# Kernel tuning notes

Hardware: AMD Instinct MI355X
Metric: run time of the kernel (lower is better)

Reference implementation:

```python
import jax, jax.numpy as jnp
import numpy as np

NUM_HEADS = 16
HEAD_DIM = 64
SCALE = 8.0 / HEAD_DIM  # use_mup=True
HGT, WID = 32, 32
EPS = 1e-5


def _layernorm(t, gamma, beta):
    # LayerNorm over last dim (head_dim)
    mu = jnp.mean(t, axis=-1, keepdims=True)
    var = jnp.var(t, axis=-1, keepdims=True)
    return (t - mu) * jax.lax.rsqrt(var + EPS) * gamma + beta


def _attention_1d(x, Wqkv, gamma, beta):
    # x: [B, N, C]; Wqkv: [3C, C] (torch Linear: y = x @ W.T)
    B, N, C = x.shape
    qkv = jnp.einsum('bnc,dc->bnd', x, Wqkv)                 # [B, N, 3C]
    qkv = qkv.reshape(B, N, 3, NUM_HEADS, HEAD_DIM)
    qkv = jnp.transpose(qkv, (2, 0, 3, 1, 4))                # [3, B, h, N, d]
    q, k, v = qkv[0], qkv[1], qkv[2]
    q = _layernorm(q, gamma, beta)
    k = _layernorm(k, gamma, beta)
    attn = jnp.einsum('bhnd,bhmd->bhnm', q * SCALE, k)       # [B, h, N, N]
    attn = jax.nn.softmax(attn, axis=-1)
    out = jnp.einsum('bhnm,bhmd->bhnd', attn, v)             # [B, h, N, d]
    return jnp.transpose(out, (0, 2, 1, 3)).reshape(B, N, C)


def setup_inputs() -> dict:
    key = jax.random.key(0)
    ks = jax.random.split(key, 3)
    B, N, C = 16, HGT * WID, 1024
    x = jax.random.normal(ks[0], (B, N, C), dtype=jnp.float32)
    Wqkv_row = jax.random.normal(ks[1], (3 * C, C), dtype=jnp.float32) * (1.0 / np.sqrt(C))
    Wqkv_col = jax.random.normal(ks[2], (3 * C, C), dtype=jnp.float32) * (1.0 / np.sqrt(C))
    return {
        'x': x,
        'Wqkv_row': Wqkv_row,
        'Wqkv_col': Wqkv_col,
        'gamma_row': jnp.ones((HEAD_DIM,), jnp.float32),
        'beta_row': jnp.zeros((HEAD_DIM,), jnp.float32),
        'gamma_col': jnp.ones((HEAD_DIM,), jnp.float32),
        'beta_col': jnp.zeros((HEAD_DIM,), jnp.float32),
    }


def reference(x, Wqkv_row, Wqkv_col, gamma_row, beta_row, gamma_col, beta_col):
    B, N, C = x.shape
    H, W = HGT, WID
    x2d = x.reshape(B, H, W, C)
    # Row attention: attend along W for every row; batch all rows together.
    rows = x2d.reshape(B * H, W, C)
    rows = _attention_1d(rows, Wqkv_row, gamma_row, beta_row)
    x2d = rows.reshape(B, H, W, C)
    # Column attention: attend along H for every column.
    cols = jnp.transpose(x2d, (0, 2, 1, 3)).reshape(B * W, H, C)
    cols = _attention_1d(cols, Wqkv_col, gamma_col, beta_col)
    x2d = jnp.transpose(cols.reshape(B, W, H, C), (0, 2, 1, 3))
    return x2d.reshape(B, N, C)
```

## Files before the change

kernel.cpp:

```cpp
#include <hip/hip_runtime.h>
#include <hip/hip_bf16.h>
#include <cstdint>

typedef _Float16 f16x8 __attribute__((ext_vector_type(8)));
typedef _Float16 f16x2 __attribute__((ext_vector_type(2)));
typedef float  f32x4  __attribute__((ext_vector_type(4)));
typedef unsigned short u16x8 __attribute__((ext_vector_type(8)));

#define GLDS(gp, lp) __builtin_amdgcn_global_load_lds( \
    (const __attribute__((address_space(1))) void*)(gp), \
    (__attribute__((address_space(3))) void*)(lp), 16, 0, 0)

static constexpr int   MROWS = 16384;
static constexpr int   N3    = 3072;
static constexpr int   NT    = 16;
static constexpr float SCALE = 0.125f;

#if __has_builtin(__builtin_amdgcn_fdot2)
#define FDOT2(a, b, c) __builtin_amdgcn_fdot2((a), (b), (c), false)
#else
__device__ __forceinline__ float FDOT2(f16x2 a, f16x2 b, float c) {
  return c + (float)a[0] * (float)b[0] + (float)a[1] * (float)b[1];
}
#endif

__device__ __forceinline__ unsigned short f2h_u(float f) {
  union { _Float16 h; unsigned short u; } c; c.h = (_Float16)f; return c.u;
}
__device__ __forceinline__ float h2f(unsigned short u) {
  union { unsigned short u; _Float16 h; } c; c.u = u; return (float)c.h;
}
__device__ __forceinline__ int permrow(int m) {
  return (m & ~1023) | ((m & 31) << 5) | ((m >> 5) & 31);
}

__global__ __launch_bounds__(256) void split_h(const float* __restrict__ src,
                                               unsigned short* __restrict__ dst) {
  int idx = blockIdx.x * 256 + threadIdx.x;
  int m = idx >> 7, k8 = (idx & 127) << 3;
  const float* s = src + (size_t)m * 1024 + k8;
  float4 v0 = *(const float4*)s;
  float4 v1 = *(const float4*)(s + 4);
  float vals[8] = {v0.x, v0.y, v0.z, v0.w, v1.x, v1.y, v1.z, v1.w};
  u16x8 hi;
#pragma unroll
  for (int i = 0; i < 8; ++i) hi[i] = f2h_u(vals[i]);
  *(u16x8*)(dst + (size_t)m * 1024 + k8) = hi;
}

__global__ __launch_bounds__(512, 2) void gemm256(const unsigned short* __restrict__ A,
                                                  const unsigned short* __restrict__ Bm,
                                                  unsigned short* __restrict__ Cq) {
  __shared__ unsigned char smem[131072];
  const int tid = threadIdx.x;
  const int w = tid >> 6, l = tid & 63;
  const int wr = w >> 2, wc = w & 3;

  const int bid = blockIdx.x;
  const int xcd = bid & 7, ic = bid >> 3;
  const int m0 = (xcd * 8 + ic / 12) << 8;
  const int n0 = (ic % 12) << 8;

  const int ske = ((l & 3) * 8) ^ ((l >= 32) ? 16 : 0);
  const unsigned short* gA0 = A  + (size_t)(m0 + w * 32 + (l >> 2)) * 1024 + ske;
  const unsigned short* gA1 = gA0 + 16 * 1024;
  const unsigned short* gB0 = Bm + (size_t)(n0 + w * 32 + (l >> 2)) * 1024 + ske;
  const unsigned short* gB1 = gB0 + 16 * 1024;
  int kT = 0;

  const int lr = l & 15;
  const int laneoff = ((lr * 64) + ((l >> 4) * 16)) ^ ((lr & 8) << 2);

#define STAGE_A(pb, kk) do { \
    GLDS(gA0 + kT + (kk) * 32, smem + (pb) * 65536 + (4 * w + (kk)) * 1024); \
    GLDS(gA1 + kT + (kk) * 32, smem + (pb) * 65536 + (4 * w + 2 + (kk)) * 1024); } while (0)
#define STAGE_B(pb, kk) do { \
    GLDS(gB0 + kT + (kk) * 32, smem + (pb) * 65536 + 32768 + (4 * w + (kk)) * 1024); \
    GLDS(gB1 + kT + (kk) * 32, smem + (pb) * 65536 + 32768 + (4 * w + 2 + (kk)) * 1024); } while (0)
#define MFMA(af, bf, c) __builtin_amdgcn_mfma_f32_16x16x32_f16(af, bf, c, 0, 0, 0)

  f32x4 acc[8][4] = {};

  STAGE_A(0, 0); STAGE_B(0, 0); STAGE_A(0, 1); STAGE_B(0, 1);
  kT = 64;
  asm volatile("s_waitcnt vmcnt(0)" ::: "memory");
  __builtin_amdgcn_s_barrier();

  for (int t = 0; t < NT; ++t) {
    const int p = t & 1, q = p ^ 1;
    const unsigned char* rb = smem + p * 65536;

    if (t < NT - 1) { STAGE_A(q, 0); STAGE_B(q, 0); STAGE_A(q, 1); STAGE_B(q, 1); }

#pragma unroll
    for (int kk = 0; kk < 2; ++kk) {
      const unsigned char* rk = rb + kk * 1024;
      f16x8 a[8], b[4];
#pragma unroll
      for (int mi = 0; mi < 8; ++mi)
        a[mi] = *(const f16x8*)(rk + (wr * 8 + mi) * 2048 + laneoff);
#pragma unroll
      for (int ni = 0; ni < 4; ++ni)
        b[ni] = *(const f16x8*)(rk + 32768 + (wc * 4 + ni) * 2048 + laneoff);
#pragma unroll
      for (int mi = 0; mi < 8; ++mi)
#pragma unroll
        for (int ni = 0; ni < 4; ++ni)
          acc[mi][ni] = MFMA(a[mi], b[ni], acc[mi][ni]);
    }

    if (t < NT - 1) {
      asm volatile("s_waitcnt vmcnt(0)" ::: "memory");
      __builtin_amdgcn_s_barrier();
    }
    kT += 64;
  }

  const int rq = (l >> 4) * 4;
#pragma unroll
  for (int mi = 0; mi < 8; ++mi)
#pragma unroll
    for (int ni = 0; ni < 4; ++ni) {
      int row = m0 + wr * 128 + mi * 16 + rq;
      int col = n0 + wc * 64 + ni * 16 + lr;
      unsigned short* cp = Cq + (size_t)row * N3 + col;
#pragma unroll
      for (int r = 0; r < 4; ++r)
        cp[(size_t)r * N3] = f2h_u(acc[mi][ni][r]);
    }
#undef STAGE_A
#undef STAGE_B
#undef MFMA
}

__global__ __launch_bounds__(256) void attn(const unsigned short* __restrict__ qkv,
                                            const float* __restrict__ gamma,
                                            const float* __restrict__ beta,
                                            float* __restrict__ out,
                                            unsigned short* __restrict__ a2,
                                            int mode) {
  __shared__ _Float16 qh[32][72];
  __shared__ _Float16 kh[32][72];
  __shared__ float v[32][68];
  __shared__ float pr[32][36];
  const int tid = threadIdx.x;
  const int s = blockIdx.x >> 4, hd = blockIdx.x & 15;
  const int p = tid >> 3, d0 = (tid & 7) * 8;
  const size_t base = (size_t)s * 32 * 3072 + hd * 64;

  {
    size_t r = base + (size_t)p * 3072 + d0;
    u16x8 qa = *(const u16x8*)(qkv + r);
    u16x8 ka = *(const u16x8*)(qkv + r + 1024);
    u16x8 va = *(const u16x8*)(qkv + r + 2048);
    float qf[8], kf[8];
    float q1 = 0.f, q2 = 0.f, k1 = 0.f, k2 = 0.f;
#pragma unroll
    for (int j = 0; j < 8; ++j) {
      qf[j] = h2f(qa[j]); kf[j] = h2f(ka[j]);
      q1 += qf[j]; q2 += qf[j] * qf[j];
      k1 += kf[j]; k2 += kf[j] * kf[j];
    }
#pragma unroll
    for (int m = 1; m <= 4; m <<= 1) {
      q1 += __shfl_xor(q1, m); q2 += __shfl_xor(q2, m);
      k1 += __shfl_xor(k1, m); k2 += __shfl_xor(k2, m);
    }
    float muq = q1 * 0.015625f, muk = k1 * 0.015625f;
    float rsq = rsqrtf(q2 * 0.015625f - muq * muq + 1e-5f);
    float rsk = rsqrtf(k2 * 0.015625f - muk * muk + 1e-5f);
    f32x4 g0 = *(const f32x4*)(gamma + d0);
    f32x4 g1 = *(const f32x4*)(gamma + d0 + 4);
    f32x4 b0 = *(const f32x4*)(beta + d0);
    f32x4 b1 = *(const f32x4*)(beta + d0 + 4);
    f16x8 qn16, kn16;
    f32x4 vv0, vv1;
#pragma unroll
    for (int j = 0; j < 8; ++j) {
      float gg = (j < 4) ? g0[j] : g1[j - 4];
      float bb = (j < 4) ? b0[j] : b1[j - 4];
      qn16[j] = (_Float16)(((qf[j] - muq) * rsq * gg + bb) * SCALE);
      kn16[j] = (_Float16)((kf[j] - muk) * rsk * gg + bb);
    }
#pragma unroll
    for (int j = 0; j < 4; ++j) { vv0[j] = h2f(va[j]); vv1[j] = h2f(va[4 + j]); }
    *(f16x8*)&qh[p][d0] = qn16;
    *(f16x8*)&kh[p][d0] = kn16;
    *(f32x4*)&v[p][d0]     = vv0;
    *(f32x4*)&v[p][d0 + 4] = vv1;
  }
  __syncthreads();

  {
    const int c0 = (tid & 7) * 4;
    float a0 = 0.f, a1 = 0.f, a2f = 0.f, a3 = 0.f;
#pragma unroll
    for (int dc = 0; dc < 8; ++dc) {
      union { f16x8 v8; f16x2 p2[4]; } qa, k0, k1, k2, k3;
      qa.v8 = *(const f16x8*)&qh[p][dc * 8];
      k0.v8 = *(const f16x8*)&kh[c0 + 0][dc * 8];
      k1.v8 = *(const f16x8*)&kh[c0 + 1][dc * 8];
      k2.v8 = *(const f16x8*)&kh[c0 + 2][dc * 8];
      k3.v8 = *(const f16x8*)&kh[c0 + 3][dc * 8];
#pragma unroll
      for (int j = 0; j < 4; ++j) {
        a0  = FDOT2(qa.p2[j], k0.p2[j], a0);
        a1  = FDOT2(qa.p2[j], k1.p2[j], a1);
        a2f = FDOT2(qa.p2[j], k2.p2[j], a2f);
        a3  = FDOT2(qa.p2[j], k3.p2[j], a3);
      }
    }
    f32x4 res; res[0] = a0; res[1] = a1; res[2] = a2f; res[3] = a3;
    *(f32x4*)&pr[p][c0] = res;
  }
  __syncthreads();

  {
    const int c0 = (tid & 7) * 4;
    f32x4 e = *(const f32x4*)&pr[p][c0];
    float mx = fmaxf(fmaxf(e[0], e[1]), fmaxf(e[2], e[3]));
#pragma unroll
    for (int m = 1; m <= 4; m <<= 1) mx = fmaxf(mx, __shfl_xor(mx, m));
    e[0] = __expf(e[0] - mx); e[1] = __expf(e[1] - mx);
    e[2] = __expf(e[2] - mx); e[3] = __expf(e[3] - mx);
    float sum = e[0] + e[1] + e[2] + e[3];
#pragma unroll
    for (int m = 1; m <= 4; m <<= 1) sum += __shfl_xor(sum, m);
    float inv = 1.f / sum;
    e[0] *= inv; e[1] *= inv; e[2] *= inv; e[3] *= inv;
    *(f32x4*)&pr[p][c0] = e;
  }
  __syncthreads();

  {
    f32x4 prr[8];
#pragma unroll
    for (int jq = 0; jq < 8; ++jq) prr[jq] = *(const f32x4*)&pr[p][jq * 4];
    f32x4 o0 = {0.f, 0.f, 0.f, 0.f}, o1 = {0.f, 0.f, 0.f, 0.f};
#pragma unroll
    for (int j = 0; j < 32; ++j) {
      float pj = prr[j >> 2][j & 3];
      f32x4 v0 = *(const f32x4*)&v[j][d0];
      f32x4 v1 = *(const f32x4*)&v[j][d0 + 4];
      o0 += pj * v0;
      o1 += pj * v1;
    }
    int pm = permrow(s * 32 + p);
    if (mode == 0) {
      u16x8 hv;
#pragma unroll
      for (int j = 0; j < 4; ++j) {
        hv[j]     = f2h_u(o0[j]);
        hv[4 + j] = f2h_u(o1[j]);
      }
      *(u16x8*)(a2 + (size_t)pm * 1024 + hd * 64 + d0) = hv;
    } else {
      float* op = out + (size_t)pm * 1024 + hd * 64 + d0;
      *(f32x4*)op       = o0;
      *(f32x4*)(op + 4) = o1;
    }
  }
}

extern "C" void kernel_launch(void* const* d_in, const int* in_sizes, int n_in,
                              void* d_out, int out_size, void* d_ws, size_t ws_size,
                              hipStream_t stream) {
  const float* x    = (const float*)d_in[0];
  const float* Wrow = (const float*)d_in[1];
  const float* Wcol = (const float*)d_in[2];
  const float* grow = (const float*)d_in[3];
  const float* brow = (const float*)d_in[4];
  const float* gcol = (const float*)d_in[5];
  const float* bcol = (const float*)d_in[6];
  float* out = (float*)d_out;

  char* ws = (char*)d_ws;
  const size_t szA2 = (size_t)MROWS * 1024 * 2;
  const size_t szB2 = (size_t)N3 * 1024 * 2;
  unsigned short* A2   = (unsigned short*)ws;
  unsigned short* B2   = (unsigned short*)(ws + szA2);
  unsigned short* qkvh = (unsigned short*)(ws + szA2 + szB2);

  split_h<<<8192, 256, 0, stream>>>(x, A2);
  split_h<<<1536, 256, 0, stream>>>(Wrow, B2);
  gemm256<<<768, 512, 0, stream>>>(A2, B2, qkvh);
  attn<<<8192, 256, 0, stream>>>(qkvh, grow, brow, out, A2, 0);
  split_h<<<1536, 256, 0, stream>>>(Wcol, B2);
  gemm256<<<768, 512, 0, stream>>>(A2, B2, qkvh);
  attn<<<8192, 256, 0, stream>>>(qkvh, gcol, bcol, out, A2, 1);
}
```

Measured before the change: 354.9 us.

## Restructure QKV GEMM into 4-slot K=32 slab ring with register double-buffering

Replaces the two-buffer 64-wide K-tile loop in the QKV projection GEMM with a four-slot ring of K=32 slabs. Global-to-LDS copies are issued two slabs ahead, and LDS fragments are double-buffered in registers so that reading the next slab overlaps the MFMAs on the current one. The XOR swizzle of the LDS layout is redesigned for the new 1 KB-per-16-row slab layout to avoid bank conflicts. The aim is to hide load latency and cut barrier stalls, at the cost of more live registers (two fragment sets) under launch bounds of 512 threads with 2 blocks.

Result: slower. 462.9 us (+30.4%).

```diff
diff --git a/kernel.cpp b/kernel.cpp
--- a/kernel.cpp
+++ b/kernel.cpp
@@ -13,7 +13,7 @@
 
 static constexpr int   MROWS = 16384;
 static constexpr int   N3    = 3072;
-static constexpr int   NT    = 16;
+static constexpr int   NSLAB = 32;
 static constexpr float SCALE = 0.125f;
 
 #if __has_builtin(__builtin_amdgcn_fdot2)
@@ -61,59 +61,67 @@
   const int m0 = (xcd * 8 + ic / 12) << 8;
   const int n0 = (ic % 12) << 8;
 
-  const int ske = ((l & 3) * 8) ^ ((l >= 32) ? 16 : 0);
+  const int ske = ((l & 3) ^ ((l >> 3) & 3)) * 8;
   const unsigned short* gA0 = A  + (size_t)(m0 + w * 32 + (l >> 2)) * 1024 + ske;
   const unsigned short* gA1 = gA0 + 16 * 1024;
   const unsigned short* gB0 = Bm + (size_t)(n0 + w * 32 + (l >> 2)) * 1024 + ske;
   const unsigned short* gB1 = gB0 + 16 * 1024;
-  int kT = 0;
 
   const int lr = l & 15;
-  const int laneoff = ((lr * 64) + ((l >> 4) * 16)) ^ ((lr & 8) << 2);
-
-#define STAGE_A(pb, kk) do { \
-    GLDS(gA0 + kT + (kk) * 32, smem + (pb) * 65536 + (4 * w + (kk)) * 1024); \
-    GLDS(gA1 + kT + (kk) * 32, smem + (pb) * 65536 + (4 * w + 2 + (kk)) * 1024); } while (0)
-#define STAGE_B(pb, kk) do { \
-    GLDS(gB0 + kT + (kk) * 32, smem + (pb) * 65536 + 32768 + (4 * w + (kk)) * 1024); \
-    GLDS(gB1 + kT + (kk) * 32, smem + (pb) * 65536 + 32768 + (4 * w + 2 + (kk)) * 1024); } while (0)
+  const int laneoff = lr * 64 + ((((l >> 4) ^ ((lr >> 1) & 3)) & 3) << 4);
+
+#define STAGE_SLAB(g) do { \
+    const int go_ = (g) * 32; \
+    unsigned char* db_ = smem + ((g) & 3) * 32768; \
+    GLDS(gA0 + go_, db_ + (2 * w) * 1024); \
+    GLDS(gA1 + go_, db_ + (2 * w + 1) * 1024); \
+    GLDS(gB0 + go_, db_ + 16384 + (2 * w) * 1024); \
+    GLDS(gB1 + go_, db_ + 16384 + (2 * w + 1) * 1024); } while (0)
 #define MFMA(af, bf, c) __builtin_amdgcn_mfma_f32_16x16x32_f16(af, bf, c, 0, 0, 0)
 
   f32x4 acc[8][4] = {};
-
-  STAGE_A(0, 0); STAGE_B(0, 0); STAGE_A(0, 1); STAGE_B(0, 1);
-  kT = 64;
+  f16x8 a0[8], b0[4], a1[8], b1[4];
+
+#define READ_SLAB(g, AS, BS) do { \
+    const unsigned char* rb_ = smem + ((g) & 3) * 32768; \
+    _Pragma("unroll") \
+    for (int mi = 0; mi < 8; ++mi) \
+      AS[mi] = *(const f16x8*)(rb_ + (wr * 8 + mi) * 1024 + laneoff); \
+    _Pragma("unroll") \
+    for (int ni = 0; ni < 4; ++ni) \
+      BS[ni] = *(const f16x8*)(rb_ + 16384 + (wc * 4 + ni) * 1024 + laneoff); } while (0)
+#define MFMA_SLAB(AS, BS) do { \
+    _Pragma("unroll") \
+    for (int mi = 0; mi < 8; ++mi) \
+      _Pragma("unroll") \
+      for (int ni = 0; ni < 4; ++ni) \
+        acc[mi][ni] = MFMA(AS[mi], BS[ni], acc[mi][ni]); } while (0)
+
+  STAGE_SLAB(0); STAGE_SLAB(1); STAGE_SLAB(2);
   asm volatile("s_waitcnt vmcnt(0)" ::: "memory");
   __builtin_amdgcn_s_barrier();
-
-  for (int t = 0; t < NT; ++t) {
-    const int p = t & 1, q = p ^ 1;
-    const unsigned char* rb = smem + p * 65536;
-
-    if (t < NT - 1) { STAGE_A(q, 0); STAGE_B(q, 0); STAGE_A(q, 1); STAGE_B(q, 1); }
-
-#pragma unroll
-    for (int kk = 0; kk < 2; ++kk) {
-      const unsigned char* rk = rb + kk * 1024;
-      f16x8 a[8], b[4];
-#pragma unroll
-      for (int mi = 0; mi < 8; ++mi)
-        a[mi] = *(const f16x8*)(rk + (wr * 8 + mi) * 2048 + laneoff);
-#pragma unroll
-      for (int ni = 0; ni < 4; ++ni)
-        b[ni] = *(const f16x8*)(rk + 32768 + (wc * 4 + ni) * 2048 + laneoff);
-#pragma unroll
-      for (int mi = 0; mi < 8; ++mi)
-#pragma unroll
-        for (int ni = 0; ni < 4; ++ni)
-          acc[mi][ni] = MFMA(a[mi], b[ni], acc[mi][ni]);
-    }
-
-    if (t < NT - 1) {
-      asm volatile("s_waitcnt vmcnt(0)" ::: "memory");
-      __builtin_amdgcn_s_barrier();
-    }
-    kT += 64;
+  READ_SLAB(0, a0, b0);
+  asm volatile("s_waitcnt lgkmcnt(0)" ::: "memory");
+  __builtin_amdgcn_s_barrier();
+
+  for (int t = 0; t < NSLAB / 2; t += 2) {
+    if (2 * t + 3 < NSLAB) STAGE_SLAB(2 * t + 3);
+    if (2 * t + 4 < NSLAB) STAGE_SLAB(2 * t + 4);
+    READ_SLAB(2 * t + 1, a1, b1);
+    MFMA_SLAB(a0, b0);
+    if (2 * t + 2 < NSLAB) READ_SLAB(2 * t + 2, a0, b0);
+    MFMA_SLAB(a1, b1);
+    asm volatile("s_waitcnt vmcnt(0) lgkmcnt(0)" ::: "memory");
+    __builtin_amdgcn_s_barrier();
+
+    if (2 * t + 5 < NSLAB) STAGE_SLAB(2 * t + 5);
+    if (2 * t + 6 < NSLAB) STAGE_SLAB(2 * t + 6);
+    READ_SLAB(2 * t + 3, a1, b1);
+    MFMA_SLAB(a0, b0);
+    if (2 * t + 4 < NSLAB) READ_SLAB(2 * t + 4, a0, b0);
+    MFMA_SLAB(a1, b1);
+    asm volatile("s_waitcnt vmcnt(0) lgkmcnt(0)" ::: "memory");
+    __builtin_amdgcn_s_barrier();
   }
 
   const int rq = (l >> 4) * 4;
@@ -128,8 +136,9 @@
       for (int r = 0; r < 4; ++r)
         cp[(size_t)r * N3] = f2h_u(acc[mi][ni][r]);
     }
-#undef STAGE_A
-#undef STAGE_B
+#undef STAGE_SLAB
+#undef READ_SLAB
+#undef MFMA_SLAB
 #undef MFMA
 }
 
```

## Halve GEMM LDS footprint with 32-wide K slabs and new swizzle

Applied to the files above, without the earlier changes.

The QKV GEMM now stages one 32-wide K slab per iteration instead of two, halving shared memory from 128KB to 64KB. The aim is to let two 512-thread blocks fit per CU as the launch bounds request. The LDS swizzle is also changed to an XOR over row bits to avoid bank conflicts with the narrower layout. The cost is twice as many barriers and waits per K, each covering less MFMA work, so latency hiding per stage is reduced.

After: 370.3 us. +4.3%, slower.

```diff
diff --git a/kernel.cpp b/kernel.cpp
--- a/kernel.cpp
+++ b/kernel.cpp
@@ -13,7 +13,7 @@
 
 static constexpr int   MROWS = 16384;
 static constexpr int   N3    = 3072;
-static constexpr int   NT    = 16;
+static constexpr int   NSLAB = 32;
 static constexpr float SCALE = 0.125f;
 
 #if __has_builtin(__builtin_amdgcn_fdot2)
@@ -51,7 +51,7 @@
 __global__ __launch_bounds__(512, 2) void gemm256(const unsigned short* __restrict__ A,
                                                   const unsigned short* __restrict__ Bm,
                                                   unsigned short* __restrict__ Cq) {
-  __shared__ unsigned char smem[131072];
+  __shared__ unsigned char smem[65536];
   const int tid = threadIdx.x;
   const int w = tid >> 6, l = tid & 63;
   const int wr = w >> 2, wc = w & 3;
@@ -61,59 +61,52 @@
   const int m0 = (xcd * 8 + ic / 12) << 8;
   const int n0 = (ic % 12) << 8;
 
-  const int ske = ((l & 3) * 8) ^ ((l >= 32) ? 16 : 0);
+  const int ske = ((l & 3) ^ ((l >> 3) & 3)) * 8;
   const unsigned short* gA0 = A  + (size_t)(m0 + w * 32 + (l >> 2)) * 1024 + ske;
   const unsigned short* gA1 = gA0 + 16 * 1024;
   const unsigned short* gB0 = Bm + (size_t)(n0 + w * 32 + (l >> 2)) * 1024 + ske;
   const unsigned short* gB1 = gB0 + 16 * 1024;
-  int kT = 0;
 
   const int lr = l & 15;
-  const int laneoff = ((lr * 64) + ((l >> 4) * 16)) ^ ((lr & 8) << 2);
-
-#define STAGE_A(pb, kk) do { \
-    GLDS(gA0 + kT + (kk) * 32, smem + (pb) * 65536 + (4 * w + (kk)) * 1024); \
-    GLDS(gA1 + kT + (kk) * 32, smem + (pb) * 65536 + (4 * w + 2 + (kk)) * 1024); } while (0)
-#define STAGE_B(pb, kk) do { \
-    GLDS(gB0 + kT + (kk) * 32, smem + (pb) * 65536 + 32768 + (4 * w + (kk)) * 1024); \
-    GLDS(gB1 + kT + (kk) * 32, smem + (pb) * 65536 + 32768 + (4 * w + 2 + (kk)) * 1024); } while (0)
+  const int laneoff = lr * 64 + ((((l >> 4) ^ ((lr >> 1) & 3)) & 3) << 4);
+
+#define STAGE_SLAB(g) do { \
+    const int go_ = (g) * 32; \
+    unsigned char* db_ = smem + ((g) & 1) * 32768; \
+    GLDS(gA0 + go_, db_ + (2 * w) * 1024); \
+    GLDS(gA1 + go_, db_ + (2 * w + 1) * 1024); \
+    GLDS(gB0 + go_, db_ + 16384 + (2 * w) * 1024); \
+    GLDS(gB1 + go_, db_ + 16384 + (2 * w + 1) * 1024); } while (0)
 #define MFMA(af, bf, c) __builtin_amdgcn_mfma_f32_16x16x32_f16(af, bf, c, 0, 0, 0)
 
   f32x4 acc[8][4] = {};
 
-  STAGE_A(0, 0); STAGE_B(0, 0); STAGE_A(0, 1); STAGE_B(0, 1);
-  kT = 64;
+  STAGE_SLAB(0);
   asm volatile("s_waitcnt vmcnt(0)" ::: "memory");
   __builtin_amdgcn_s_barrier();
 
-  for (int t = 0; t < NT; ++t) {
-    const int p = t & 1, q = p ^ 1;
-    const unsigned char* rb = smem + p * 65536;
-
-    if (t < NT - 1) { STAGE_A(q, 0); STAGE_B(q, 0); STAGE_A(q, 1); STAGE_B(q, 1); }
-
-#pragma unroll
-    for (int kk = 0; kk < 2; ++kk) {
-      const unsigned char* rk = rb + kk * 1024;
-      f16x8 a[8], b[4];
-#pragma unroll
-      for (int mi = 0; mi < 8; ++mi)
-        a[mi] = *(const f16x8*)(rk + (wr * 8 + mi) * 2048 + laneoff);
+  for (int g = 0; g < NSLAB; ++g) {
+    const unsigned char* rb = smem + (g & 1) * 32768;
+
+    if (g < NSLAB - 1) STAGE_SLAB(g + 1);
+
+    f16x8 a[8], b[4];
+#pragma unroll
+    for (int mi = 0; mi < 8; ++mi)
+      a[mi] = *(const f16x8*)(rb + (wr * 8 + mi) * 1024 + laneoff);
+#pragma unroll
+    for (int ni = 0; ni < 4; ++ni)
+      b[ni] = *(const f16x8*)(rb + 16384 + (wc * 4 + ni) * 1024 + laneoff);
+#pragma unroll
+    for (int mi = 0; mi < 8; ++mi)
 #pragma unroll
       for (int ni = 0; ni < 4; ++ni)
-        b[ni] = *(const f16x8*)(rk + 32768 + (wc * 4 + ni) * 2048 + laneoff);
-#pragma unroll
-      for (int mi = 0; mi < 8; ++mi)
-#pragma unroll
-        for (int ni = 0; ni < 4; ++ni)
-          acc[mi][ni] = MFMA(a[mi], b[ni], acc[mi][ni]);
-    }
-
-    if (t < NT - 1) {
-      asm volatile("s_waitcnt vmcnt(0)" ::: "memory");
+        acc[mi][ni] = MFMA(a[mi], b[ni], acc[mi][ni]);
+
+    if (g < NSLAB - 1) {
+      asm volatile("s_waitcnt vmcnt(0) lgkmcnt(0)" ::: "memory");
       __builtin_amdgcn_s_barrier();
     }
-    kT += 64;
   }
 
   const int rq = (l >> 4) * 4;
@@ -128,8 +121,7 @@
       for (int r = 0; r < 4; ++r)
         cp[(size_t)r * N3] = f2h_u(acc[mi][ni][r]);
     }
-#undef STAGE_A
-#undef STAGE_B
+#undef STAGE_SLAB
 #undef MFMA
 }
 
```
